# Kernel optimization log

Measured on AMD Instinct MI355X. Metric: run time of the kernel, lower is better.

The kernel has to match this reference:

```python
import jax, jax.numpy as jnp
import numpy as np

B, T, D, H = 16, 4096, 128, 256


def setup_inputs() -> dict:
    key = jax.random.key(0)
    k0, k1, k2 = jax.random.split(key, 3)
    inputs = jax.random.normal(k0, (B, T, D), dtype=jnp.float32)
    # Kaiming-uniform-ish scaling like nn.Linear defaults (std ~ 1/sqrt(fan_in))
    W_x = jax.random.normal(k1, (H, D), dtype=jnp.float32) * (1.0 / np.sqrt(D))
    W_h = jax.random.normal(k2, (H, H), dtype=jnp.float32) * (1.0 / np.sqrt(H))
    b_x = jnp.zeros((H,), dtype=jnp.float32)
    b_h = jnp.zeros((H,), dtype=jnp.float32)
    return {"inputs": inputs, "W_x": W_x, "b_x": b_x, "W_h": W_h, "b_h": b_h}


def reference(inputs, W_x, b_x, W_h, b_h):
    # Precompute x2h for all timesteps at once (one big GEMM): [B, T, H]
    xh = jnp.einsum('btd,hd->bth', inputs, W_x) + b_x
    h0 = jnp.zeros((inputs.shape[0], W_h.shape[0]), dtype=inputs.dtype)

    def step(h, xt):
        # h_t = tanh(x2h(x_t) + h2h(h_{t-1}))
        h_new = jnp.tanh(xt + h @ W_h.T + b_h)
        return h_new, h_new

    # scan over time axis: xh transposed to [T, B, H]
    _, hs = jax.lax.scan(step, h0, jnp.swapaxes(xh, 0, 1))
    # hiddens returned as [B, T, H] (matches permute(1,0,2) of stacked states)
    return jnp.swapaxes(hs, 0, 1)
```

## Files before the change

kernel.cpp:

```cpp
#include <hip/hip_runtime.h>

typedef _Float16 f16x8 __attribute__((ext_vector_type(8)));
typedef float f32x4 __attribute__((ext_vector_type(4)));

#define BB 16
#define TT 4096
#define DD 128
#define HH 256

__device__ __forceinline__ float tanh_fast(float x) {
    float e = __expf(2.0f * x);
    return 1.0f - 2.0f * __builtin_amdgcn_rcpf(e + 1.0f);
}

__global__ __launch_bounds__(256) void x2h_gemm(
    const float* __restrict__ inp, const float* __restrict__ Wx,
    const float* __restrict__ bx, float* __restrict__ out)
{
    const int tid = threadIdx.x;
    const int ty = tid >> 4, tx = tid & 15;
    const int row0 = blockIdx.x * 128 + ty * 8;
    const int col0 = blockIdx.y * 128 + tx * 8;

    float acc[8][8] = {};

    #pragma unroll 2
    for (int k4 = 0; k4 < DD / 4; ++k4) {
        float4 a[8], b[8];
        #pragma unroll
        for (int r = 0; r < 8; ++r)
            a[r] = *(const float4*)&inp[(size_t)(row0 + r) * DD + k4 * 4];
        #pragma unroll
        for (int c = 0; c < 8; ++c)
            b[c] = *(const float4*)&Wx[(size_t)(col0 + c) * DD + k4 * 4];
        #pragma unroll
        for (int r = 0; r < 8; ++r)
            #pragma unroll
            for (int c = 0; c < 8; ++c)
                acc[r][c] += a[r].x * b[c].x + a[r].y * b[c].y
                           + a[r].z * b[c].z + a[r].w * b[c].w;
    }

    float4 bx0 = *(const float4*)&bx[col0];
    float4 bx1 = *(const float4*)&bx[col0 + 4];
    #pragma unroll
    for (int r = 0; r < 8; ++r) {
        float4 o0, o1;
        o0.x = acc[r][0] + bx0.x; o0.y = acc[r][1] + bx0.y;
        o0.z = acc[r][2] + bx0.z; o0.w = acc[r][3] + bx0.w;
        o1.x = acc[r][4] + bx1.x; o1.y = acc[r][5] + bx1.y;
        o1.z = acc[r][6] + bx1.z; o1.w = acc[r][7] + bx1.w;
        *(float4*)&out[(size_t)(row0 + r) * HH + col0]     = o0;
        *(float4*)&out[(size_t)(row0 + r) * HH + col0 + 4] = o1;
    }
}

__global__ __launch_bounds__(256, 1) void rnn_scan(
    const float* __restrict__ Wh, const float* __restrict__ bh,
    float* __restrict__ out)
{
    const int tid  = threadIdx.x;
    const int w    = tid >> 6;
    const int lane = tid & 63;
    const int g    = lane >> 4;
    const int c    = lane & 15;
    const int b    = blockIdx.x;
    const int j    = (w << 6) + lane;

    __shared__ __align__(16) _Float16 hbuf[2][HH];

    f16x8 wb[4][8];
    #pragma unroll
    for (int T = 0; T < 4; ++T) {
        const float* wrow = Wh + (size_t)((w << 6) + (T << 4) + c) * HH;
        #pragma unroll
        for (int t = 0; t < 8; ++t) {
            const float* wp = wrow + (t << 5) + (g << 3);
            float4 v0 = *(const float4*)wp;
            float4 v1 = *(const float4*)(wp + 4);
            wb[T][t] = f16x8{(_Float16)v0.x, (_Float16)v0.y,
                             (_Float16)v0.z, (_Float16)v0.w,
                             (_Float16)v1.x, (_Float16)v1.y,
                             (_Float16)v1.z, (_Float16)v1.w};
        }
    }
    const float bhv = bh[j];
    hbuf[0][tid] = (_Float16)0.f;

    float* colp = out + (size_t)b * TT * HH + j;

    constexpr int CH = 8;
    float xc[CH], xn[CH];
    #pragma unroll
    for (int i = 0; i < CH; ++i) xc[i] = colp[(size_t)i * HH];
    __syncthreads();

    const int abase = (g << 4);

    int cur = 0;
    const int NC = TT / CH;
    for (int cch = 0; cch < NC; ++cch) {
        if (cch + 1 < NC) {
            const float* p = colp + (size_t)(cch + 1) * CH * HH;
            #pragma unroll
            for (int i = 0; i < CH; ++i) xn[i] = p[(size_t)i * HH];
        }
        float* op = colp + (size_t)cch * CH * HH;
        #pragma unroll
        for (int s = 0; s < CH; ++s) {
            const char* hb = (const char*)hbuf[cur];
            uint4 hv0 = *(const uint4*)(hb + 0 * 64 + abase);
            uint4 hv1 = *(const uint4*)(hb + 1 * 64 + abase);
            uint4 hv2 = *(const uint4*)(hb + 2 * 64 + abase);
            uint4 hv3 = *(const uint4*)(hb + 3 * 64 + abase);
            uint4 hv4 = *(const uint4*)(hb + 4 * 64 + abase);
            uint4 hv5 = *(const uint4*)(hb + 5 * 64 + abase);
            uint4 hv6 = *(const uint4*)(hb + 6 * 64 + abase);
            uint4 hv7 = *(const uint4*)(hb + 7 * 64 + abase);
            f16x8 a0 = __builtin_bit_cast(f16x8, hv0);
            f16x8 a1 = __builtin_bit_cast(f16x8, hv1);
            f16x8 a2 = __builtin_bit_cast(f16x8, hv2);
            f16x8 a3 = __builtin_bit_cast(f16x8, hv3);
            f16x8 a4 = __builtin_bit_cast(f16x8, hv4);
            f16x8 a5 = __builtin_bit_cast(f16x8, hv5);
            f16x8 a6 = __builtin_bit_cast(f16x8, hv6);
            f16x8 a7 = __builtin_bit_cast(f16x8, hv7);

            f32x4 acc0 = {0.f, 0.f, 0.f, 0.f};
            f32x4 acc1 = {0.f, 0.f, 0.f, 0.f};
            f32x4 acc2 = {0.f, 0.f, 0.f, 0.f};
            f32x4 acc3 = {0.f, 0.f, 0.f, 0.f};
#define MF(ACC, T, AV, TI) \
            ACC = __builtin_amdgcn_mfma_f32_16x16x32_f16(AV, wb[T][TI], ACC, 0, 0, 0);
            MF(acc0, 0, a0, 0) MF(acc1, 1, a0, 0) MF(acc2, 2, a0, 0) MF(acc3, 3, a0, 0)
            MF(acc0, 0, a1, 1) MF(acc1, 1, a1, 1) MF(acc2, 2, a1, 1) MF(acc3, 3, a1, 1)
            MF(acc0, 0, a2, 2) MF(acc1, 1, a2, 2) MF(acc2, 2, a2, 2) MF(acc3, 3, a2, 2)
            MF(acc0, 0, a3, 3) MF(acc1, 1, a3, 3) MF(acc2, 2, a3, 3) MF(acc3, 3, a3, 3)
            MF(acc0, 0, a4, 4) MF(acc1, 1, a4, 4) MF(acc2, 2, a4, 4) MF(acc3, 3, a4, 4)
            MF(acc0, 0, a5, 5) MF(acc1, 1, a5, 5) MF(acc2, 2, a5, 5) MF(acc3, 3, a5, 5)
            MF(acc0, 0, a6, 6) MF(acc1, 1, a6, 6) MF(acc2, 2, a6, 6) MF(acc3, 3, a6, 6)
            MF(acc0, 0, a7, 7) MF(acc1, 1, a7, 7) MF(acc2, 2, a7, 7) MF(acc3, 3, a7, 7)
#undef MF
            float av = acc0[0];
            av = (g == 1) ? acc1[0] : av;
            av = (g == 2) ? acc2[0] : av;
            av = (g == 3) ? acc3[0] : av;

            float z  = xc[s] + bhv + av;
            float hn = tanh_fast(z);
            op[(size_t)s * HH] = hn;
            hbuf[cur ^ 1][j] = (_Float16)hn;
            cur ^= 1;
            __syncthreads();
        }
        #pragma unroll
        for (int i = 0; i < CH; ++i) xc[i] = xn[i];
    }
}

extern "C" void kernel_launch(void* const* d_in, const int* in_sizes, int n_in,
                              void* d_out, int out_size, void* d_ws, size_t ws_size,
                              hipStream_t stream) {
    const float* inp = (const float*)d_in[0];
    const float* Wx  = (const float*)d_in[1];
    const float* bx  = (const float*)d_in[2];
    const float* Wh  = (const float*)d_in[3];
    const float* bh  = (const float*)d_in[4];
    float* out = (float*)d_out;

    dim3 g1(BB * TT / 128, HH / 128);
    x2h_gemm<<<g1, 256, 0, stream>>>(inp, Wx, bx, out);
    rnn_scan<<<BB, 256, 0, stream>>>(Wh, bh, out);
}
```

Measured before the change: 1.793 ms.

## Split recurrent matvec K-dimension across two wave groups with LDS reduction

The scan block grows from 256 to 512 threads, and each pair of waves splits the 256-wide hidden reduction into two halves. Each wave now issues 16 MFMAs per step instead of 32, shortening the serial latency chain. Partial sums go to shared memory and are combined by the first 256 threads before tanh. The cost is a second __syncthreads per timestep and an extra LDS round trip, which may cancel the shorter MFMA chain.

```diff
diff --git a/kernel.cpp b/kernel.cpp
--- a/kernel.cpp
+++ b/kernel.cpp
@@ -55,7 +55,7 @@
     }
 }
 
-__global__ __launch_bounds__(256, 1) void rnn_scan(
+__global__ __launch_bounds__(512, 2) void rnn_scan(
     const float* __restrict__ Wh, const float* __restrict__ bh,
     float* __restrict__ out)
 {
@@ -64,17 +64,19 @@
     const int lane = tid & 63;
     const int g    = lane >> 4;
     const int c    = lane & 15;
+    const int kh   = w & 1;
+    const int nq   = w >> 1;
     const int b    = blockIdx.x;
-    const int j    = (w << 6) + lane;
 
     __shared__ __align__(16) _Float16 hbuf[2][HH];
+    __shared__ __align__(16) float     part[2][HH];
 
-    f16x8 wb[4][8];
+    f16x8 wb[4][4];
     #pragma unroll
     for (int T = 0; T < 4; ++T) {
-        const float* wrow = Wh + (size_t)((w << 6) + (T << 4) + c) * HH;
+        const float* wrow = Wh + (size_t)((nq << 6) + (T << 4) + c) * HH + (kh << 7);
         #pragma unroll
-        for (int t = 0; t < 8; ++t) {
+        for (int t = 0; t < 4; ++t) {
             const float* wp = wrow + (t << 5) + (g << 3);
             float4 v0 = *(const float4*)wp;
             float4 v1 = *(const float4*)(wp + 4);
@@ -84,23 +86,31 @@
                              (_Float16)v1.z, (_Float16)v1.w};
         }
     }
-    const float bhv = bh[j];
-    hbuf[0][tid] = (_Float16)0.f;
 
-    float* colp = out + (size_t)b * TT * HH + j;
+    const int jp = (nq << 6) + (g << 4) + c;
+
+    float bhv = 0.f;
+    float* colp = nullptr;
+    if (tid < HH) {
+        bhv  = bh[tid];
+        colp = out + (size_t)b * TT * HH + tid;
+        hbuf[0][tid] = (_Float16)0.f;
+    }
 
     constexpr int CH = 8;
     float xc[CH], xn[CH];
-    #pragma unroll
-    for (int i = 0; i < CH; ++i) xc[i] = colp[(size_t)i * HH];
+    if (tid < HH) {
+        #pragma unroll
+        for (int i = 0; i < CH; ++i) xc[i] = colp[(size_t)i * HH];
+    }
     __syncthreads();
 
-    const int abase = (g << 4);
+    const int abase = (kh << 8) + (g << 4);
 
     int cur = 0;
     const int NC = TT / CH;
     for (int cch = 0; cch < NC; ++cch) {
-        if (cch + 1 < NC) {
+        if (tid < HH && cch + 1 < NC) {
             const float* p = colp + (size_t)(cch + 1) * CH * HH;
             #pragma unroll
             for (int i = 0; i < CH; ++i) xn[i] = p[(size_t)i * HH];
@@ -109,22 +119,14 @@
         #pragma unroll
         for (int s = 0; s < CH; ++s) {
             const char* hb = (const char*)hbuf[cur];
-            uint4 hv0 = *(const uint4*)(hb + 0 * 64 + abase);
-            uint4 hv1 = *(const uint4*)(hb + 1 * 64 + abase);
-            uint4 hv2 = *(const uint4*)(hb + 2 * 64 + abase);
-            uint4 hv3 = *(const uint4*)(hb + 3 * 64 + abase);
-            uint4 hv4 = *(const uint4*)(hb + 4 * 64 + abase);
-            uint4 hv5 = *(const uint4*)(hb + 5 * 64 + abase);
-            uint4 hv6 = *(const uint4*)(hb + 6 * 64 + abase);
-            uint4 hv7 = *(const uint4*)(hb + 7 * 64 + abase);
+            uint4 hv0 = *(const uint4*)(hb + abase + 0 * 64);
+            uint4 hv1 = *(const uint4*)(hb + abase + 1 * 64);
+            uint4 hv2 = *(const uint4*)(hb + abase + 2 * 64);
+            uint4 hv3 = *(const uint4*)(hb + abase + 3 * 64);
             f16x8 a0 = __builtin_bit_cast(f16x8, hv0);
             f16x8 a1 = __builtin_bit_cast(f16x8, hv1);
             f16x8 a2 = __builtin_bit_cast(f16x8, hv2);
             f16x8 a3 = __builtin_bit_cast(f16x8, hv3);
-            f16x8 a4 = __builtin_bit_cast(f16x8, hv4);
-            f16x8 a5 = __builtin_bit_cast(f16x8, hv5);
-            f16x8 a6 = __builtin_bit_cast(f16x8, hv6);
-            f16x8 a7 = __builtin_bit_cast(f16x8, hv7);
 
             f32x4 acc0 = {0.f, 0.f, 0.f, 0.f};
             f32x4 acc1 = {0.f, 0.f, 0.f, 0.f};
@@ -136,25 +138,27 @@
             MF(acc0, 0, a1, 1) MF(acc1, 1, a1, 1) MF(acc2, 2, a1, 1) MF(acc3, 3, a1, 1)
             MF(acc0, 0, a2, 2) MF(acc1, 1, a2, 2) MF(acc2, 2, a2, 2) MF(acc3, 3, a2, 2)
             MF(acc0, 0, a3, 3) MF(acc1, 1, a3, 3) MF(acc2, 2, a3, 3) MF(acc3, 3, a3, 3)
-            MF(acc0, 0, a4, 4) MF(acc1, 1, a4, 4) MF(acc2, 2, a4, 4) MF(acc3, 3, a4, 4)
-            MF(acc0, 0, a5, 5) MF(acc1, 1, a5, 5) MF(acc2, 2, a5, 5) MF(acc3, 3, a5, 5)
-            MF(acc0, 0, a6, 6) MF(acc1, 1, a6, 6) MF(acc2, 2, a6, 6) MF(acc3, 3, a6, 6)
-            MF(acc0, 0, a7, 7) MF(acc1, 1, a7, 7) MF(acc2, 2, a7, 7) MF(acc3, 3, a7, 7)
 #undef MF
-            float av = acc0[0];
-            av = (g == 1) ? acc1[0] : av;
-            av = (g == 2) ? acc2[0] : av;
-            av = (g == 3) ? acc3[0] : av;
+            float v = acc0[0];
+            v = (g == 1) ? acc1[0] : v;
+            v = (g == 2) ? acc2[0] : v;
+            v = (g == 3) ? acc3[0] : v;
+            part[kh][jp] = v;
+            __syncthreads();
 
-            float z  = xc[s] + bhv + av;
-            float hn = tanh_fast(z);
-            op[(size_t)s * HH] = hn;
-            hbuf[cur ^ 1][j] = (_Float16)hn;
+            if (tid < HH) {
+                float z  = xc[s] + bhv + part[0][tid] + part[1][tid];
+                float hn = tanh_fast(z);
+                op[(size_t)s * HH] = hn;
+                hbuf[cur ^ 1][tid] = (_Float16)hn;
+            }
             cur ^= 1;
             __syncthreads();
         }
-        #pragma unroll
-        for (int i = 0; i < CH; ++i) xc[i] = xn[i];
+        if (tid < HH) {
+            #pragma unroll
+            for (int i = 0; i < CH; ++i) xc[i] = xn[i];
+        }
     }
 }
 
@@ -170,5 +174,5 @@
 
     dim3 g1(BB * TT / 128, HH / 128);
     x2h_gemm<<<g1, 256, 0, stream>>>(inp, Wx, bx, out);
-    rnn_scan<<<BB, 256, 0, stream>>>(Wh, bh, out);
+    rnn_scan<<<BB, 512, 0, stream>>>(Wh, bh, out);
 }
```

After: 1.992 ms. +11.1%, slower.
